# Optimization experiments

Measured on AMD Instinct MI355X. Metric: run time of the kernel, lower is better.

Reference implementation:

```python
import jax, jax.numpy as jnp
import numpy as np

B, S, D, H = 4, 2048, 1024, 16
DH = D // H


def setup_inputs() -> dict:
    key = jax.random.key(0)
    ks = jax.random.split(key, 5)
    std = 1.0 / np.sqrt(D)
    return {
        "x": jax.random.normal(ks[0], (B, S, D), dtype=jnp.float32),
        "mask": jnp.ones((S, S), dtype=bool),  # unused by the original forward
        "Wq": jax.random.normal(ks[1], (D, D), dtype=jnp.float32) * std,
        "Wk": jax.random.normal(ks[2], (D, D), dtype=jnp.float32) * std,
        "Wv": jax.random.normal(ks[3], (D, D), dtype=jnp.float32) * std,
        "Wout": jax.random.normal(ks[4], (D, D), dtype=jnp.float32) * std,
    }


def reference(x, mask, Wq, Wk, Wv, Wout):
    n, s, d = x.shape
    scale = 1.0 / np.sqrt(DH).astype(np.float32)
    q = (x @ Wq).reshape(n, s, H, DH)
    k = (x @ Wk).reshape(n, s, H, DH)
    v = (x @ Wv).reshape(n, s, H, DH)
    # scores [n, q, k, h]; softmax over k axis (dim=-2 in original)
    attn = jnp.einsum('nqhd,nkhd->nqkh', q, k) * scale
    attn = jax.nn.softmax(attn, axis=-2)
    z = jnp.einsum('nqkh,nkhd->nqhd', attn, v).reshape(n, s, d)
    z = jnp.einsum('nqd,de->nqe', z, Wout)
    return x + z
```

## Files before the change

### kernel.cpp

```cpp
#include <hip/hip_runtime.h>

#define Bn 4
#define Sn 2048
#define Dn 1024
#define Hn 16
#define DHn 64

typedef float f32x4 __attribute__((ext_vector_type(4)));
typedef short bf16x8 __attribute__((ext_vector_type(8)));
typedef unsigned short u16;
typedef unsigned int u32;
typedef unsigned short u16x8 __attribute__((ext_vector_type(8)));
typedef unsigned short u16x4 __attribute__((ext_vector_type(4)));
typedef u32 u32x4 __attribute__((ext_vector_type(4)));

union B8 { u32x4 u; bf16x8 s; u16x8 h; };

__device__ __forceinline__ u16 f2bf(float f){
  union { float f; u32 u; } v; v.f = f;
  return (u16)((v.u + 0x7fffu + ((v.u >> 16) & 1u)) >> 16);
}

__device__ __forceinline__ u32 pack_bf2(float lo, float hi){
  union { float f; u32 u; } a, b;
  a.f = lo; b.f = hi;
  return __builtin_amdgcn_perm(b.u, a.u, 0x07060302u);
}

#if __has_builtin(__builtin_amdgcn_exp2f)
#define EXP2(x) __builtin_amdgcn_exp2f(x)
#define QSCALE 0.18033688011112042f
#else
#define EXP2(x) __expf(x)
#define QSCALE 0.125f
#endif

#if __has_builtin(__builtin_amdgcn_global_load_lds)
#define G2L16(l, g) __builtin_amdgcn_global_load_lds((const __attribute__((address_space(1))) u32*)(g), \
                                                     (__attribute__((address_space(3))) u32*)(l), 16, 0, 0)
#else
#define G2L16(l, g) (*(bf16x8*)(l) = *(const bf16x8*)(g))
#endif

__global__ void prep_kernel(const float* __restrict__ x,
                            const float* __restrict__ Wq, const float* __restrict__ Wk,
                            const float* __restrict__ Wv, const float* __restrict__ Wo,
                            u16* __restrict__ xb, u16* __restrict__ wt_all){
  __shared__ u16 tile[64*66];
  const int t = threadIdx.x;
  if (blockIdx.x < 4096){
    size_t i = ((size_t)blockIdx.x * 256 + t) * 8;
    float4 f0 = *(const float4*)(x + i);
    float4 f1 = *(const float4*)(x + i + 4);
    u16x8 o;
    o[0]=f2bf(f0.x); o[1]=f2bf(f0.y); o[2]=f2bf(f0.z); o[3]=f2bf(f0.w);
    o[4]=f2bf(f1.x); o[5]=f2bf(f1.y); o[6]=f2bf(f1.z); o[7]=f2bf(f1.w);
    *(u16x8*)(xb + i) = o;
    return;
  }
  const int wi = blockIdx.x - 4096;
  const int z = wi >> 8, r8 = wi & 255;
  const int k0 = (r8 >> 4) * 64, n0 = (r8 & 15) * 64;
  const float* w = (z == 0) ? Wq : (z == 1) ? Wk : (z == 2) ? Wv : Wo;
  const float scale = (z == 0) ? QSCALE : 1.0f;
  u16* wt = wt_all + (size_t)z * Dn * Dn;
  #pragma unroll
  for (int i = 0; i < 4; i++){
    int idx = i*256 + t;
    int r = idx >> 4, c4 = (idx & 15) * 4;
    float4 f = *(const float4*)(w + (size_t)(k0 + r)*Dn + n0 + c4);
    tile[r*66 + c4 + 0] = f2bf(f.x * scale);
    tile[r*66 + c4 + 1] = f2bf(f.y * scale);
    tile[r*66 + c4 + 2] = f2bf(f.z * scale);
    tile[r*66 + c4 + 3] = f2bf(f.w * scale);
  }
  __syncthreads();
  #pragma unroll
  for (int i = 0; i < 4; i++){
    int idx = i*256 + t;
    int nr = idx >> 4, kc4 = (idx & 15) * 4;
    u16x4 o;
    o[0] = tile[(kc4+0)*66 + nr];
    o[1] = tile[(kc4+1)*66 + nr];
    o[2] = tile[(kc4+2)*66 + nr];
    o[3] = tile[(kc4+3)*66 + nr];
    *(u16x4*)(wt + (size_t)(n0 + nr)*Dn + k0 + kc4) = o;
  }
}

__launch_bounds__(256)
__global__ void gemm_qkv_kernel(const u16* __restrict__ xb, const u16* __restrict__ wt_all,
                                u16* __restrict__ qb, u16* __restrict__ kb, u16* __restrict__ vtb){
  __shared__ u16 smem[32768];
  const int t = threadIdx.x;
  const int wave = t >> 6, lane = t & 63;
  const int ln = lane & 15, quad = lane >> 4;
  const int wm = wave >> 1, wn = wave & 1;
  const int n0 = blockIdx.x * 128;
  const int m0 = blockIdx.y * 128;
  const int zsel = blockIdx.z;
  const u16* wt = wt_all + (size_t)zsel * Dn * Dn;

  f32x4 acc[4][4] = {};

  #pragma unroll
  for (int sub = 0; sub < 2; sub++)
    #pragma unroll
    for (int i = 0; i < 2; i++){
      int idx = i*256 + t;
      int r = idx >> 2, c8 = (idx & 3) * 8;
      G2L16(&smem[sub*8192 + idx*8],        xb + (size_t)(m0 + r)*Dn + sub*32 + c8);
      G2L16(&smem[sub*8192 + 4096 + idx*8], wt + (size_t)(n0 + r)*Dn + sub*32 + c8);
    }

  for (int ki = 0; ki < 16; ki++){
    const int cur = ki & 1;
    __syncthreads();
    if (ki + 1 < 16){
      const int nxt = 16384 * ((ki+1) & 1);
      const int kt = (ki+1) * 64;
      #pragma unroll
      for (int sub = 0; sub < 2; sub++)
        #pragma unroll
        for (int i = 0; i < 2; i++){
          int idx = i*256 + t;
          int r = idx >> 2, c8 = (idx & 3) * 8;
          G2L16(&smem[nxt + sub*8192 + idx*8],        xb + (size_t)(m0 + r)*Dn + kt + sub*32 + c8);
          G2L16(&smem[nxt + sub*8192 + 4096 + idx*8], wt + (size_t)(n0 + r)*Dn + kt + sub*32 + c8);
        }
    }
    #pragma unroll
    for (int sub = 0; sub < 2; sub++){
      const u16* As = &smem[16384*cur + sub*8192];
      const u16* Bs = As + 4096;
      bf16x8 a[4], b[4];
      #pragma unroll
      for (int rb = 0; rb < 4; rb++) a[rb] = *(const bf16x8*)&As[(wm*64 + rb*16 + ln)*32 + quad*8];
      #pragma unroll
      for (int cb = 0; cb < 4; cb++) b[cb] = *(const bf16x8*)&Bs[(wn*64 + cb*16 + ln)*32 + quad*8];
      #pragma unroll
      for (int rb = 0; rb < 4; rb++)
        #pragma unroll
        for (int cb = 0; cb < 4; cb++)
          acc[rb][cb] = __builtin_amdgcn_mfma_f32_16x16x32_bf16(a[rb], b[cb], acc[rb][cb], 0, 0, 0);
    }
  }

  __syncthreads();
  u16* Cs = smem;
  if (zsel < 2){
    #pragma unroll
    for (int rb = 0; rb < 4; rb++)
      #pragma unroll
      for (int cb = 0; cb < 4; cb++)
        #pragma unroll
        for (int reg = 0; reg < 4; reg++)
          Cs[(wm*64 + rb*16 + quad*4 + reg)*136 + wn*64 + cb*16 + ln] = f2bf(acc[rb][cb][reg]);
  } else {
    #pragma unroll
    for (int rb = 0; rb < 4; rb++)
      #pragma unroll
      for (int cb = 0; cb < 4; cb++){
        u16x4 o;
        #pragma unroll
        for (int reg = 0; reg < 4; reg++) o[reg] = f2bf(acc[rb][cb][reg]);
        *(u16x4*)&Cs[(wn*64 + cb*16 + ln)*136 + wm*64 + rb*16 + quad*4] = o;
      }
  }
  __syncthreads();

  if (zsel < 2){
    u16* outp = (zsel == 0) ? qb : kb;
    #pragma unroll
    for (int i = 0; i < 8; i++){
      int idx = i*256 + t;
      int r = idx >> 4, c8 = (idx & 15) * 8;
      bf16x8 vdat = *(const bf16x8*)&Cs[r*136 + c8];
      int row = m0 + r, bb = row >> 11, s = row & 2047;
      int col = n0 + c8, hh = col >> 6, d = col & 63;
      *(bf16x8*)(outp + (((size_t)bb*Hn + hh)*Sn + s)*DHn + d) = vdat;
    }
  } else {
    #pragma unroll
    for (int i = 0; i < 8; i++){
      int idx = i*256 + t;
      int c = idx >> 4, r8 = (idx & 15) * 8;
      bf16x8 vdat = *(const bf16x8*)&Cs[c*136 + r8];
      int col = n0 + c, hh = col >> 6, d = col & 63;
      int row = m0 + r8, bb = row >> 11, s = row & 2047;
      *(bf16x8*)(vtb + (((size_t)bb*Hn + hh)*DHn + d)*Sn + s) = vdat;
    }
  }
}

__launch_bounds__(256, 2)
__global__ void attn_kernel(const u16* q, const u16* __restrict__ k,
                            const u16* __restrict__ vt, u16* z){
  __shared__ u16 Ks[2][64*72];
  __shared__ u16 Vs[2][64*72];
  const int t = threadIdx.x;
  const int wave = t >> 6, lane = t & 63;
  const int ln = lane & 15, quad = lane >> 4;
  const int qt = blockIdx.x, h = blockIdx.y, b = blockIdx.z;
  const size_t bh = (size_t)b * Hn + h;
  const int q0 = qt*256 + wave*64;
  const u16* qp = q + bh * Sn * DHn;
  const u16* kp = k + bh * Sn * DHn;
  const u16* vp = vt + bh * DHn * Sn;

  bf16x8 qf[4][2];
  #pragma unroll
  for (int n = 0; n < 4; n++)
    #pragma unroll
    for (int kq = 0; kq < 2; kq++)
      qf[n][kq] = *(const bf16x8*)(qp + (size_t)(q0 + n*16 + ln)*DHn + kq*32 + quad*8);

  f32x4 zacc[4][4] = {};
  float dacc[4] = {0.f, 0.f, 0.f, 0.f};

  int sr[2], sc[2], vc1[2], vc2[2];
  #pragma unroll
  for (int i = 0; i < 2; i++){
    int idx = i*256 + t, r = idx >> 3, a = idx & 7;
    sr[i] = r; sc[i] = a*8;
    int ksg = a >> 2, q1 = ((a&3)*2)&3, h1 = (a&3) >> 1;
    vc1[i] = ksg*32 + q1*8 + h1*4;
    vc2[i] = ksg*32 + (((q1+1)&3))*8 + h1*4;
  }

  bf16x8 rk[2], rv[2];
  #pragma unroll
  for (int i = 0; i < 2; i++){
    rk[i] = *(const bf16x8*)(kp + (size_t)sr[i]*DHn + sc[i]);
    rv[i] = *(const bf16x8*)(vp + (size_t)sr[i]*Sn + sc[i]);
  }
  #pragma unroll
  for (int i = 0; i < 2; i++){
    *(bf16x8*)&Ks[0][sr[i]*72 + sc[i]] = rk[i];
    u16x4 lo = *(u16x4*)&rv[i];
    u16x4 hi = *((u16x4*)&rv[i] + 1);
    *(u16x4*)&Vs[0][sr[i]*72 + vc1[i]] = lo;
    *(u16x4*)&Vs[0][sr[i]*72 + vc2[i]] = hi;
  }

  for (int kt = 0; kt < Sn/64; kt++){
    const int cur = kt & 1;
    __syncthreads();

    if (kt + 1 < Sn/64){
      #pragma unroll
      for (int i = 0; i < 2; i++){
        rk[i] = *(const bf16x8*)(kp + (size_t)((kt+1)*64 + sr[i])*DHn + sc[i]);
        rv[i] = *(const bf16x8*)(vp + (size_t)sr[i]*Sn + (kt+1)*64 + sc[i]);
      }
    }
    const u16* Kc = Ks[cur];
    const u16* Vc = Vs[cur];

    #pragma unroll
    for (int ks = 0; ks < 2; ks++){
      f32x4 sacc[2][4] = {};
      #pragma unroll
      for (int kq = 0; kq < 2; kq++){
        bf16x8 ka[2];
        #pragma unroll
        for (int m2 = 0; m2 < 2; m2++)
          ka[m2] = *(const bf16x8*)&Kc[((2*ks + m2)*16 + ln)*72 + kq*32 + quad*8];
        #pragma unroll
        for (int m2 = 0; m2 < 2; m2++)
          #pragma unroll
          for (int n = 0; n < 4; n++)
            sacc[m2][n] = __builtin_amdgcn_mfma_f32_16x16x32_bf16(ka[m2], qf[n][kq], sacc[m2][n], 0, 0, 0);
      }
      B8 pb[4];
      #pragma unroll
      for (int n = 0; n < 4; n++){
        f32x4 s0 = sacc[0][n], s1 = sacc[1][n];
        float a0 = EXP2(s0[0]), a1 = EXP2(s0[1]), a2 = EXP2(s0[2]), a3 = EXP2(s0[3]);
        float b0 = EXP2(s1[0]), b1 = EXP2(s1[1]), b2 = EXP2(s1[2]), b3 = EXP2(s1[3]);
        dacc[n] += ((a0 + a1) + (a2 + a3)) + ((b0 + b1) + (b2 + b3));
        pb[n].u = (u32x4){pack_bf2(a0, a1), pack_bf2(a2, a3), pack_bf2(b0, b1), pack_bf2(b2, b3)};
      }
      #pragma unroll
      for (int mtd = 0; mtd < 4; mtd++){
        bf16x8 va = *(const bf16x8*)&Vc[(mtd*16 + ln)*72 + ks*32 + quad*8];
        #pragma unroll
        for (int n = 0; n < 4; n++)
          zacc[mtd][n] = __builtin_amdgcn_mfma_f32_16x16x32_bf16(va, pb[n].s, zacc[mtd][n], 0, 0, 0);
      }
    }

    if (kt + 1 < Sn/64){
      const int nxt = (kt+1) & 1;
      #pragma unroll
      for (int i = 0; i < 2; i++){
        *(bf16x8*)&Ks[nxt][sr[i]*72 + sc[i]] = rk[i];
        u16x4 lo = *(u16x4*)&rv[i];
        u16x4 hi = *((u16x4*)&rv[i] + 1);
        *(u16x4*)&Vs[nxt][sr[i]*72 + vc1[i]] = lo;
        *(u16x4*)&Vs[nxt][sr[i]*72 + vc2[i]] = hi;
      }
    }
  }

  float inv[4];
  #pragma unroll
  for (int n = 0; n < 4; n++){
    float d = dacc[n];
    d += __shfl_xor(d, 16, 64);
    d += __shfl_xor(d, 32, 64);
    inv[n] = 1.0f / d;
  }

  #pragma unroll
  for (int mtd = 0; mtd < 4; mtd++)
    #pragma unroll
    for (int n = 0; n < 4; n++){
      u16x4 o;
      #pragma unroll
      for (int j = 0; j < 4; j++) o[j] = f2bf(zacc[mtd][n][j] * inv[n]);
      *(u16x4*)(z + (bh*Sn + (size_t)(q0 + n*16 + ln))*DHn + mtd*16 + quad*4) = o;
    }
}

__launch_bounds__(256)
__global__ void gemm_out_kernel(const u16* __restrict__ zb, const u16* __restrict__ wt,
                                const float* __restrict__ x, float* __restrict__ out){
  __shared__ u16 smem[32768];
  const int t = threadIdx.x;
  const int wave = t >> 6, lane = t & 63;
  const int ln = lane & 15, quad = lane >> 4;
  const int wm = wave >> 1, wn = wave & 1;
  const int n0 = blockIdx.x * 128;
  const int m0 = blockIdx.y * 128;

  f32x4 acc[4][4] = {};

  #pragma unroll
  for (int sub = 0; sub < 2; sub++)
    #pragma unroll
    for (int i = 0; i < 2; i++){
      int idx = i*256 + t;
      int r = idx >> 2, c8 = (idx & 3) * 8;
      int row = m0 + r, bb = row >> 11, s = row & 2047;
      G2L16(&smem[sub*8192 + idx*8],        zb + (((size_t)bb*Hn + 0)*Sn + s)*DHn + sub*32 + c8);
      G2L16(&smem[sub*8192 + 4096 + idx*8], wt + (size_t)(n0 + r)*Dn + sub*32 + c8);
    }

  for (int ki = 0; ki < 16; ki++){
    const int cur = ki & 1;
    __syncthreads();
    if (ki + 1 < 16){
      const int nxt = 16384 * ((ki+1) & 1);
      const int hh = ki + 1;
      const int kt = (ki+1) * 64;
      #pragma unroll
      for (int sub = 0; sub < 2; sub++)
        #pragma unroll
        for (int i = 0; i < 2; i++){
          int idx = i*256 + t;
          int r = idx >> 2, c8 = (idx & 3) * 8;
          int row = m0 + r, bb = row >> 11, s = row & 2047;
          G2L16(&smem[nxt + sub*8192 + idx*8],        zb + (((size_t)bb*Hn + hh)*Sn + s)*DHn + sub*32 + c8);
          G2L16(&smem[nxt + sub*8192 + 4096 + idx*8], wt + (size_t)(n0 + r)*Dn + kt + sub*32 + c8);
        }
    }
    #pragma unroll
    for (int sub = 0; sub < 2; sub++){
      const u16* As = &smem[16384*cur + sub*8192];
      const u16* Bs = As + 4096;
      bf16x8 a[4], b[4];
      #pragma unroll
      for (int rb = 0; rb < 4; rb++) a[rb] = *(const bf16x8*)&As[(wm*64 + rb*16 + ln)*32 + quad*8];
      #pragma unroll
      for (int cb = 0; cb < 4; cb++) b[cb] = *(const bf16x8*)&Bs[(wn*64 + cb*16 + ln)*32 + quad*8];
      #pragma unroll
      for (int rb = 0; rb < 4; rb++)
        #pragma unroll
        for (int cb = 0; cb < 4; cb++)
          acc[rb][cb] = __builtin_amdgcn_mfma_f32_16x16x32_bf16(a[rb], b[cb], acc[rb][cb], 0, 0, 0);
    }
  }

  #pragma unroll
  for (int rb = 0; rb < 4; rb++)
    #pragma unroll
    for (int cb = 0; cb < 4; cb++)
      #pragma unroll
      for (int reg = 0; reg < 4; reg++){
        int row = m0 + wm*64 + rb*16 + quad*4 + reg;
        int col = n0 + wn*64 + cb*16 + ln;
        size_t off = (size_t)row*Dn + col;
        out[off] = acc[rb][cb][reg] + x[off];
      }
}

extern "C" void kernel_launch(void* const* d_in, const int* in_sizes, int n_in,
                              void* d_out, int out_size, void* d_ws, size_t ws_size,
                              hipStream_t stream){
  const float* x    = (const float*)d_in[0];
  const float* Wq   = (const float*)d_in[2];
  const float* Wk   = (const float*)d_in[3];
  const float* Wv   = (const float*)d_in[4];
  const float* Wout = (const float*)d_in[5];
  float* out = (float*)d_out;

  u16* ws = (u16*)d_ws;
  const size_t NW = (size_t)Dn * Dn;
  const size_t NX = (size_t)Bn * Sn * Dn;
  u16* wt  = ws;
  u16* xb  = wt + 4*NW;
  u16* qb  = xb + NX;
  u16* kb  = qb + NX;
  u16* vtb = kb + NX;

  dim3 blk(256);
  prep_kernel     <<<dim3(4096 + 1024), blk, 0, stream>>>(x, Wq, Wk, Wv, Wout, xb, wt);
  gemm_qkv_kernel <<<dim3(8,64,3), blk, 0, stream>>>(xb, wt, qb, kb, vtb);
  attn_kernel     <<<dim3(8,16,4), blk, 0, stream>>>(qb, kb, vtb, qb);
  gemm_out_kernel <<<dim3(8,64), blk, 0, stream>>>(qb, wt + 3*NW, x, out);
}
```

Baseline: 279.0 us.

## Rewrite QKV GEMM with 256x256 tiles, swizzled LDS and interleaved prefetch schedule

The QKV projection GEMM moves to 512-thread workgroups computing 256x256 output tiles. It uses XOR-swizzled LDS layouts and a hand-scheduled pipeline that interleaves half-tile global-to-LDS loads with MFMA phases, using raw barriers, vmcnt waits and setprio. Workgroup IDs are remapped across XCDs for the QKV, attention and output GEMM kernels to improve L2 locality. The larger tiles cut global traffic per FLOP but raise register and LDS pressure. The manual waitcnt and barrier scheduling is fragile.

```diff
diff --git a/kernel.cpp b/kernel.cpp
--- a/kernel.cpp
+++ b/kernel.cpp
@@ -88,107 +88,193 @@
   }
 }
 
-__launch_bounds__(256)
+#define MFMA_B16(d, va, vb) (d) = __builtin_amdgcn_mfma_f32_16x16x32_bf16((va), (vb), (d), 0, 0, 0)
+#define BARRAW() __builtin_amdgcn_s_barrier()
+#define WAIT_LGKM0() asm volatile("s_waitcnt lgkmcnt(0)" ::: "memory")
+#define VM6() asm volatile("s_waitcnt vmcnt(6)" ::: "memory")
+#define VM0() asm volatile("s_waitcnt vmcnt(0)" ::: "memory")
+#define SCHEDB() __builtin_amdgcn_sched_barrier(0)
+
+__launch_bounds__(512, 2)
 __global__ void gemm_qkv_kernel(const u16* __restrict__ xb, const u16* __restrict__ wt_all,
                                 u16* __restrict__ qb, u16* __restrict__ kb, u16* __restrict__ vtb){
-  __shared__ u16 smem[32768];
+  __shared__ u16 sm[65536];
   const int t = threadIdx.x;
-  const int wave = t >> 6, lane = t & 63;
+  const int lane = t & 63, wave = t >> 6;
   const int ln = lane & 15, quad = lane >> 4;
-  const int wm = wave >> 1, wn = wave & 1;
-  const int n0 = blockIdx.x * 128;
-  const int m0 = blockIdx.y * 128;
-  const int zsel = blockIdx.z;
+  const int wm = wave >> 2, wn = wave & 3;
+
+  const int lin = blockIdx.x;
+  const int wg = (lin & 7) * 48 + (lin >> 3);
+  const int zsel = wg >> 7;
+  const int rem = wg & 127;
+  const int m0 = (rem >> 2) * 256;
+  const int n0 = (rem & 3) * 256;
   const u16* wt = wt_all + (size_t)zsel * Dn * Dn;
 
-  f32x4 acc[4][4] = {};
-
-  #pragma unroll
-  for (int sub = 0; sub < 2; sub++)
-    #pragma unroll
-    for (int i = 0; i < 2; i++){
-      int idx = i*256 + t;
-      int r = idx >> 2, c8 = (idx & 3) * 8;
-      G2L16(&smem[sub*8192 + idx*8],        xb + (size_t)(m0 + r)*Dn + sub*32 + c8);
-      G2L16(&smem[sub*8192 + 4096 + idx*8], wt + (size_t)(n0 + r)*Dn + sub*32 + c8);
-    }
-
-  for (int ki = 0; ki < 16; ki++){
-    const int cur = ki & 1;
-    __syncthreads();
-    if (ki + 1 < 16){
-      const int nxt = 16384 * ((ki+1) & 1);
-      const int kt = (ki+1) * 64;
-      #pragma unroll
-      for (int sub = 0; sub < 2; sub++)
-        #pragma unroll
-        for (int i = 0; i < 2; i++){
-          int idx = i*256 + t;
-          int r = idx >> 2, c8 = (idx & 3) * 8;
-          G2L16(&smem[nxt + sub*8192 + idx*8],        xb + (size_t)(m0 + r)*Dn + kt + sub*32 + c8);
-          G2L16(&smem[nxt + sub*8192 + 4096 + idx*8], wt + (size_t)(n0 + r)*Dn + kt + sub*32 + c8);
+  const int r0 = t >> 3,      sg0 = (t & 7) ^ (r0 & 7);
+  const int i1 = 512 + t;
+  const int r1 = i1 >> 3,     sg1 = (i1 & 7) ^ (r1 & 7);
+  const u16* ax0 = xb + (size_t)(m0 + r0)*Dn + sg0*8;
+  const u16* ax1 = xb + (size_t)(m0 + r1)*Dn + sg1*8;
+  const u16* bw0 = wt + (size_t)(n0 + r0)*Dn + sg0*8;
+  const u16* bw1 = wt + (size_t)(n0 + r1)*Dn + sg1*8;
+  const int ld0 = t*8, ld1 = 4096 + t*8;
+
+#define STG_A(buf, h, tt) do { \
+    G2L16(&sm[(buf)*32768 + (h)*8192 + ld0], ax0 + (size_t)(h)*128*Dn + (tt)*64); \
+    G2L16(&sm[(buf)*32768 + (h)*8192 + ld1], ax1 + (size_t)(h)*128*Dn + (tt)*64); } while(0)
+#define STG_B(buf, h, tt) do { \
+    G2L16(&sm[(buf)*32768 + 16384 + (h)*8192 + ld0], bw0 + (size_t)(h)*128*Dn + (tt)*64); \
+    G2L16(&sm[(buf)*32768 + 16384 + (h)*8192 + ld1], bw1 + (size_t)(h)*128*Dn + (tt)*64); } while(0)
+
+  const int swz = (ln & 7) * 8;
+  const int ac0 = (quad*8) ^ swz;
+  const int ac1 = (32 + quad*8) ^ swz;
+  const int abase = wm*8192 + ln*64;
+  const int bbase = 16384 + (wn>>1)*8192 + ((wn&1)*64 + ln)*64;
+
+  f32x4 acc[8][4] = {};
+  bf16x8 aq[4][2], bq[4][2];
+
+  STG_B(0,0,0); STG_B(0,1,0); STG_A(0,0,0); STG_A(0,1,0);
+  STG_B(1,0,1); STG_B(1,1,1); STG_A(1,0,1);
+  VM6();
+  BARRAW();
+
+  for (int tp = 0; tp < 16; tp += 2){
+    #pragma unroll
+    for (int pi2 = 0; pi2 < 2; pi2++){
+      const int tt = tp + pi2;
+      const int cur = pi2;
+      const int nxt = cur ^ 1;
+      const u16* bufp = &sm[cur*32768];
+
+      #pragma unroll
+      for (int i = 0; i < 4; i++){
+        aq[i][0] = *(const bf16x8*)&bufp[abase + i*1024 + ac0];
+        aq[i][1] = *(const bf16x8*)&bufp[abase + i*1024 + ac1];
+      }
+      #pragma unroll
+      for (int nf = 0; nf < 4; nf++){
+        bq[nf][0] = *(const bf16x8*)&bufp[bbase + nf*1024 + ac0];
+        bq[nf][1] = *(const bf16x8*)&bufp[bbase + nf*1024 + ac1];
+      }
+      SCHEDB();
+      if (tt + 1 < 16) STG_A(nxt, 1, tt+1);
+      BARRAW();
+      WAIT_LGKM0();
+      __builtin_amdgcn_s_setprio(1);
+      #pragma unroll
+      for (int i = 0; i < 4; i++)
+        #pragma unroll
+        for (int nf = 0; nf < 2; nf++){
+          MFMA_B16(acc[i][nf], aq[i][0], bq[nf][0]);
+          MFMA_B16(acc[i][nf], aq[i][1], bq[nf][1]);
         }
-    }
-    #pragma unroll
-    for (int sub = 0; sub < 2; sub++){
-      const u16* As = &smem[16384*cur + sub*8192];
-      const u16* Bs = As + 4096;
-      bf16x8 a[4], b[4];
-      #pragma unroll
-      for (int rb = 0; rb < 4; rb++) a[rb] = *(const bf16x8*)&As[(wm*64 + rb*16 + ln)*32 + quad*8];
-      #pragma unroll
-      for (int cb = 0; cb < 4; cb++) b[cb] = *(const bf16x8*)&Bs[(wn*64 + cb*16 + ln)*32 + quad*8];
-      #pragma unroll
-      for (int rb = 0; rb < 4; rb++)
-        #pragma unroll
-        for (int cb = 0; cb < 4; cb++)
-          acc[rb][cb] = __builtin_amdgcn_mfma_f32_16x16x32_bf16(a[rb], b[cb], acc[rb][cb], 0, 0, 0);
-    }
-  }
-
-  __syncthreads();
-  u16* Cs = smem;
-  if (zsel < 2){
-    #pragma unroll
-    for (int rb = 0; rb < 4; rb++)
-      #pragma unroll
-      for (int cb = 0; cb < 4; cb++)
-        #pragma unroll
-        for (int reg = 0; reg < 4; reg++)
-          Cs[(wm*64 + rb*16 + quad*4 + reg)*136 + wn*64 + cb*16 + ln] = f2bf(acc[rb][cb][reg]);
-  } else {
-    #pragma unroll
-    for (int rb = 0; rb < 4; rb++)
-      #pragma unroll
-      for (int cb = 0; cb < 4; cb++){
-        u16x4 o;
-        #pragma unroll
-        for (int reg = 0; reg < 4; reg++) o[reg] = f2bf(acc[rb][cb][reg]);
-        *(u16x4*)&Cs[(wn*64 + cb*16 + ln)*136 + wm*64 + rb*16 + quad*4] = o;
-      }
-  }
-  __syncthreads();
-
+      __builtin_amdgcn_s_setprio(0);
+      BARRAW();
+
+      if (tt + 2 < 16) STG_B(cur, 0, tt+2);
+      BARRAW();
+      __builtin_amdgcn_s_setprio(1);
+      #pragma unroll
+      for (int i = 0; i < 4; i++)
+        #pragma unroll
+        for (int nf = 2; nf < 4; nf++){
+          MFMA_B16(acc[i][nf], aq[i][0], bq[nf][0]);
+          MFMA_B16(acc[i][nf], aq[i][1], bq[nf][1]);
+        }
+      __builtin_amdgcn_s_setprio(0);
+      BARRAW();
+
+      #pragma unroll
+      for (int i = 0; i < 4; i++){
+        aq[i][0] = *(const bf16x8*)&bufp[abase + (4+i)*1024 + ac0];
+        aq[i][1] = *(const bf16x8*)&bufp[abase + (4+i)*1024 + ac1];
+      }
+      SCHEDB();
+      if (tt + 2 < 16) STG_B(cur, 1, tt+2);
+      BARRAW();
+      WAIT_LGKM0();
+      __builtin_amdgcn_s_setprio(1);
+      #pragma unroll
+      for (int i = 0; i < 4; i++)
+        #pragma unroll
+        for (int nf = 2; nf < 4; nf++){
+          MFMA_B16(acc[4+i][nf], aq[i][0], bq[nf][0]);
+          MFMA_B16(acc[4+i][nf], aq[i][1], bq[nf][1]);
+        }
+      __builtin_amdgcn_s_setprio(0);
+      BARRAW();
+
+      if (tt + 2 < 16) STG_A(cur, 0, tt+2);
+      BARRAW();
+      __builtin_amdgcn_s_setprio(1);
+      #pragma unroll
+      for (int i = 0; i < 4; i++)
+        #pragma unroll
+        for (int nf = 0; nf < 2; nf++){
+          MFMA_B16(acc[4+i][nf], aq[i][0], bq[nf][0]);
+          MFMA_B16(acc[4+i][nf], aq[i][1], bq[nf][1]);
+        }
+      __builtin_amdgcn_s_setprio(0);
+      if (tt + 2 < 16) { VM6(); } else { VM0(); }
+      BARRAW();
+    }
+  }
+
+  u16* Cs = sm;
   if (zsel < 2){
     u16* outp = (zsel == 0) ? qb : kb;
     #pragma unroll
-    for (int i = 0; i < 8; i++){
-      int idx = i*256 + t;
-      int r = idx >> 4, c8 = (idx & 15) * 8;
-      bf16x8 vdat = *(const bf16x8*)&Cs[r*136 + c8];
-      int row = m0 + r, bb = row >> 11, s = row & 2047;
-      int col = n0 + c8, hh = col >> 6, d = col & 63;
-      *(bf16x8*)(outp + (((size_t)bb*Hn + hh)*Sn + s)*DHn + d) = vdat;
+    for (int round = 0; round < 2; round++){
+      if (wm == round){
+        #pragma unroll
+        for (int mf = 0; mf < 8; mf++)
+          #pragma unroll
+          for (int nf = 0; nf < 4; nf++)
+            #pragma unroll
+            for (int reg = 0; reg < 4; reg++)
+              Cs[(mf*16 + quad*4 + reg)*264 + wn*64 + nf*16 + ln] = f2bf(acc[mf][nf][reg]);
+      }
+      __syncthreads();
+      #pragma unroll
+      for (int it = 0; it < 8; it++){
+        int idx = it*512 + t;
+        int r = idx >> 5, c8 = (idx & 31) * 8;
+        bf16x8 vdat = *(const bf16x8*)&Cs[r*264 + c8];
+        int row = m0 + round*128 + r, bb = row >> 11, s = row & 2047;
+        int col = n0 + c8, hh = col >> 6, d = col & 63;
+        *(bf16x8*)(outp + (((size_t)bb*Hn + hh)*Sn + s)*DHn + d) = vdat;
+      }
+      if (round == 0) __syncthreads();
     }
   } else {
     #pragma unroll
-    for (int i = 0; i < 8; i++){
-      int idx = i*256 + t;
-      int c = idx >> 4, r8 = (idx & 15) * 8;
-      bf16x8 vdat = *(const bf16x8*)&Cs[c*136 + r8];
-      int col = n0 + c, hh = col >> 6, d = col & 63;
-      int row = m0 + r8, bb = row >> 11, s = row & 2047;
-      *(bf16x8*)(vtb + (((size_t)bb*Hn + hh)*DHn + d)*Sn + s) = vdat;
+    for (int round = 0; round < 2; round++){
+      if ((wn >> 1) == round){
+        #pragma unroll
+        for (int mf = 0; mf < 8; mf++)
+          #pragma unroll
+          for (int nf = 0; nf < 4; nf++){
+            u16x4 o;
+            #pragma unroll
+            for (int reg = 0; reg < 4; reg++) o[reg] = f2bf(acc[mf][nf][reg]);
+            *(u16x4*)&Cs[((wn&1)*64 + nf*16 + ln)*264 + wm*128 + mf*16 + quad*4] = o;
+          }
+      }
+      __syncthreads();
+      #pragma unroll
+      for (int it = 0; it < 8; it++){
+        int idx = it*512 + t;
+        int r = idx >> 5, c8 = (idx & 31) * 8;
+        bf16x8 vdat = *(const bf16x8*)&Cs[r*264 + c8];
+        int col = n0 + round*128 + r, hh = col >> 6, d = col & 63;
+        int row = m0 + c8, bb = row >> 11, s = row & 2047;
+        *(bf16x8*)(vtb + (((size_t)bb*Hn + hh)*DHn + d)*Sn + s) = vdat;
+      }
+      if (round == 0) __syncthreads();
     }
   }
 }
@@ -201,7 +287,9 @@
   const int t = threadIdx.x;
   const int wave = t >> 6, lane = t & 63;
   const int ln = lane & 15, quad = lane >> 4;
-  const int qt = blockIdx.x, h = blockIdx.y, b = blockIdx.z;
+  const int lin = blockIdx.x + 8*(blockIdx.y + 16*blockIdx.z);
+  const int wgs = (lin & 7)*64 + (lin >> 3);
+  const int qt = wgs & 7, h = (wgs >> 3) & 15, b = wgs >> 7;
   const size_t bh = (size_t)b * Hn + h;
   const int q0 = qt*256 + wave*64;
   const u16* qp = q + bh * Sn * DHn;
@@ -331,8 +419,10 @@
   const int wave = t >> 6, lane = t & 63;
   const int ln = lane & 15, quad = lane >> 4;
   const int wm = wave >> 1, wn = wave & 1;
-  const int n0 = blockIdx.x * 128;
-  const int m0 = blockIdx.y * 128;
+  const int lin = blockIdx.y * 8 + blockIdx.x;
+  const int wgs = (lin & 7)*64 + (lin >> 3);
+  const int n0 = (wgs & 7) * 128;
+  const int m0 = (wgs >> 3) * 128;
 
   f32x4 acc[4][4] = {};
 
@@ -414,9 +504,8 @@
   u16* kb  = qb + NX;
   u16* vtb = kb + NX;
 
-  dim3 blk(256);
-  prep_kernel     <<<dim3(4096 + 1024), blk, 0, stream>>>(x, Wq, Wk, Wv, Wout, xb, wt);
-  gemm_qkv_kernel <<<dim3(8,64,3), blk, 0, stream>>>(xb, wt, qb, kb, vtb);
-  attn_kernel     <<<dim3(8,16,4), blk, 0, stream>>>(qb, kb, vtb, qb);
-  gemm_out_kernel <<<dim3(8,64), blk, 0, stream>>>(qb, wt + 3*NW, x, out);
-}
+  prep_kernel     <<<dim3(4096 + 1024), dim3(256), 0, stream>>>(x, Wq, Wk, Wv, Wout, xb, wt);
+  gemm_qkv_kernel <<<dim3(384), dim3(512), 0, stream>>>(xb, wt, qb, kb, vtb);
+  attn_kernel     <<<dim3(8,16,4), dim3(256), 0, stream>>>(qb, kb, vtb, qb);
+  gemm_out_kernel <<<dim3(8,64), dim3(256), 0, stream>>>(qb, wt + 3*NW, x, out);
+}
```

New measurement: 263.7 us. 1.06x faster.

## Rework GEMM pipelines with swizzled LDS, triple buffering, and XCD-aware block remapping

Applied to the files above, without the earlier changes.

Both projection GEMMs are rewritten so the A tile is triple-buffered and the B tile double-buffered in LDS. Loads use an XOR-swizzled 64-wide layout to avoid bank conflicts. Explicit vmcnt/lgkmcnt waits, raw barriers, sched_barriers and setprio interleave the global-to-LDS prefetch with the MFMA work. Block indices for the GEMMs and the attention kernel are remapped so consecutive workgroups land on the same XCD, aiming for better L2 reuse. The hand-written wait counts and barriers are fragile and raise LDS use per block.

```diff
diff --git a/kernel.cpp b/kernel.cpp
--- a/kernel.cpp
+++ b/kernel.cpp
@@ -41,6 +41,13 @@
 #else
 #define G2L16(l, g) (*(bf16x8*)(l) = *(const bf16x8*)(g))
 #endif
+
+#define MFMA_B16(d, va, vb) (d) = __builtin_amdgcn_mfma_f32_16x16x32_bf16((va), (vb), (d), 0, 0, 0)
+#define BARRAW() __builtin_amdgcn_s_barrier()
+#define WAIT_LGKM0() asm volatile("s_waitcnt lgkmcnt(0)" ::: "memory")
+#define VM4() asm volatile("s_waitcnt vmcnt(4)" ::: "memory")
+#define VM0() asm volatile("s_waitcnt vmcnt(0)" ::: "memory")
+#define SCHEDB() __builtin_amdgcn_sched_barrier(0)
 
 __global__ void prep_kernel(const float* __restrict__ x,
                             const float* __restrict__ Wq, const float* __restrict__ Wk,
@@ -91,64 +98,106 @@
 __launch_bounds__(256)
 __global__ void gemm_qkv_kernel(const u16* __restrict__ xb, const u16* __restrict__ wt_all,
                                 u16* __restrict__ qb, u16* __restrict__ kb, u16* __restrict__ vtb){
-  __shared__ u16 smem[32768];
+  __shared__ u16 sm[40960];
   const int t = threadIdx.x;
-  const int wave = t >> 6, lane = t & 63;
+  const int lane = t & 63, wave = t >> 6;
   const int ln = lane & 15, quad = lane >> 4;
   const int wm = wave >> 1, wn = wave & 1;
-  const int n0 = blockIdx.x * 128;
-  const int m0 = blockIdx.y * 128;
-  const int zsel = blockIdx.z;
+
+  const int lin = blockIdx.x;
+  const int wg = (lin & 7) * 192 + (lin >> 3);
+  const int zsel = wg >> 9;
+  const int rem = wg & 511;
+  const int m0 = (rem >> 3) * 128;
+  const int n0 = (rem & 7) * 128;
   const u16* wt = wt_all + (size_t)zsel * Dn * Dn;
 
+  const u16* ap[4]; const u16* bp[4]; int ldo[4];
+  #pragma unroll
+  for (int p = 0; p < 4; p++){
+    int idx = p*256 + t;
+    int r = idx >> 3, g = (idx & 7) ^ (r & 7);
+    ap[p] = xb + (size_t)(m0 + r)*Dn + g*8;
+    bp[p] = wt + (size_t)(n0 + r)*Dn + g*8;
+    ldo[p] = idx * 8;
+  }
+#define STGA(buf, tt) do { _Pragma("unroll") for (int p = 0; p < 4; p++) \
+    G2L16(&sm[(buf) + ldo[p]], ap[p] + (size_t)(tt)*64); } while(0)
+#define STGB(buf, tt) do { _Pragma("unroll") for (int p = 0; p < 4; p++) \
+    G2L16(&sm[(buf) + ldo[p]], bp[p] + (size_t)(tt)*64); } while(0)
+
+  const int agr0 = ((    quad) ^ (ln & 7)) * 8;
+  const int agr1 = ((4 + quad) ^ (ln & 7)) * 8;
+  int arow[4], brow[4];
+  #pragma unroll
+  for (int i = 0; i < 4; i++) arow[i] = (wm*64 + i*16 + ln) * 64;
+  #pragma unroll
+  for (int j = 0; j < 4; j++) brow[j] = (wn*64 + j*16 + ln) * 64;
+
   f32x4 acc[4][4] = {};
 
-  #pragma unroll
-  for (int sub = 0; sub < 2; sub++)
+  STGA(0, 0); STGB(24576, 0); STGA(8192, 1);
+
+  #pragma unroll
+  for (int tt = 0; tt < 16; ++tt){
+    const int a_cur = (tt % 3) * 8192;
+    const int a_pf  = ((tt + 2) % 3) * 8192;
+    const int b_cur = 24576 + (tt & 1) * 8192;
+    const int b_pf  = 24576 + ((tt + 1) & 1) * 8192;
+
+    if (tt < 15) { VM4(); } else { VM0(); }
+    BARRAW(); SCHEDB();
+
+    bf16x8 a01[2][2], bq[4][2];
     #pragma unroll
     for (int i = 0; i < 2; i++){
-      int idx = i*256 + t;
-      int r = idx >> 2, c8 = (idx & 3) * 8;
-      G2L16(&smem[sub*8192 + idx*8],        xb + (size_t)(m0 + r)*Dn + sub*32 + c8);
-      G2L16(&smem[sub*8192 + 4096 + idx*8], wt + (size_t)(n0 + r)*Dn + sub*32 + c8);
-    }
-
-  for (int ki = 0; ki < 16; ki++){
-    const int cur = ki & 1;
-    __syncthreads();
-    if (ki + 1 < 16){
-      const int nxt = 16384 * ((ki+1) & 1);
-      const int kt = (ki+1) * 64;
-      #pragma unroll
-      for (int sub = 0; sub < 2; sub++)
-        #pragma unroll
-        for (int i = 0; i < 2; i++){
-          int idx = i*256 + t;
-          int r = idx >> 2, c8 = (idx & 3) * 8;
-          G2L16(&smem[nxt + sub*8192 + idx*8],        xb + (size_t)(m0 + r)*Dn + kt + sub*32 + c8);
-          G2L16(&smem[nxt + sub*8192 + 4096 + idx*8], wt + (size_t)(n0 + r)*Dn + kt + sub*32 + c8);
-        }
-    }
-    #pragma unroll
-    for (int sub = 0; sub < 2; sub++){
-      const u16* As = &smem[16384*cur + sub*8192];
-      const u16* Bs = As + 4096;
-      bf16x8 a[4], b[4];
-      #pragma unroll
-      for (int rb = 0; rb < 4; rb++) a[rb] = *(const bf16x8*)&As[(wm*64 + rb*16 + ln)*32 + quad*8];
-      #pragma unroll
-      for (int cb = 0; cb < 4; cb++) b[cb] = *(const bf16x8*)&Bs[(wn*64 + cb*16 + ln)*32 + quad*8];
-      #pragma unroll
-      for (int rb = 0; rb < 4; rb++)
-        #pragma unroll
-        for (int cb = 0; cb < 4; cb++)
-          acc[rb][cb] = __builtin_amdgcn_mfma_f32_16x16x32_bf16(a[rb], b[cb], acc[rb][cb], 0, 0, 0);
-    }
+      a01[i][0] = *(const bf16x8*)&sm[a_cur + arow[i] + agr0];
+      a01[i][1] = *(const bf16x8*)&sm[a_cur + arow[i] + agr1];
+    }
+    #pragma unroll
+    for (int j = 0; j < 4; j++){
+      bq[j][0] = *(const bf16x8*)&sm[b_cur + brow[j] + agr0];
+      bq[j][1] = *(const bf16x8*)&sm[b_cur + brow[j] + agr1];
+    }
+    SCHEDB();
+    if (tt < 15) STGB(b_pf, tt + 1);
+    SCHEDB();
+    WAIT_LGKM0(); SCHEDB();
+    __builtin_amdgcn_s_setprio(1);
+    #pragma unroll
+    for (int i = 0; i < 2; i++)
+      #pragma unroll
+      for (int j = 0; j < 4; j++){
+        MFMA_B16(acc[i][j], a01[i][0], bq[j][0]);
+        MFMA_B16(acc[i][j], a01[i][1], bq[j][1]);
+      }
+    __builtin_amdgcn_s_setprio(0);
+
+    bf16x8 a23[2][2];
+    #pragma unroll
+    for (int i = 0; i < 2; i++){
+      a23[i][0] = *(const bf16x8*)&sm[a_cur + arow[2+i] + agr0];
+      a23[i][1] = *(const bf16x8*)&sm[a_cur + arow[2+i] + agr1];
+    }
+    SCHEDB();
+    if (tt < 14) STGA(a_pf, tt + 2);
+    SCHEDB();
+    WAIT_LGKM0(); SCHEDB();
+    __builtin_amdgcn_s_setprio(1);
+    #pragma unroll
+    for (int i = 0; i < 2; i++)
+      #pragma unroll
+      for (int j = 0; j < 4; j++){
+        MFMA_B16(acc[2+i][j], a23[i][0], bq[j][0]);
+        MFMA_B16(acc[2+i][j], a23[i][1], bq[j][1]);
+      }
+    __builtin_amdgcn_s_setprio(0);
   }
 
   __syncthreads();
-  u16* Cs = smem;
+  u16* Cs = sm;
   if (zsel < 2){
+    u16* outp = (zsel == 0) ? qb : kb;
     #pragma unroll
     for (int rb = 0; rb < 4; rb++)
       #pragma unroll
@@ -156,21 +205,7 @@
         #pragma unroll
         for (int reg = 0; reg < 4; reg++)
           Cs[(wm*64 + rb*16 + quad*4 + reg)*136 + wn*64 + cb*16 + ln] = f2bf(acc[rb][cb][reg]);
-  } else {
-    #pragma unroll
-    for (int rb = 0; rb < 4; rb++)
-      #pragma unroll
-      for (int cb = 0; cb < 4; cb++){
-        u16x4 o;
-        #pragma unroll
-        for (int reg = 0; reg < 4; reg++) o[reg] = f2bf(acc[rb][cb][reg]);
-        *(u16x4*)&Cs[(wn*64 + cb*16 + ln)*136 + wm*64 + rb*16 + quad*4] = o;
-      }
-  }
-  __syncthreads();
-
-  if (zsel < 2){
-    u16* outp = (zsel == 0) ? qb : kb;
+    __syncthreads();
     #pragma unroll
     for (int i = 0; i < 8; i++){
       int idx = i*256 + t;
@@ -182,6 +217,16 @@
     }
   } else {
     #pragma unroll
+    for (int rb = 0; rb < 4; rb++)
+      #pragma unroll
+      for (int cb = 0; cb < 4; cb++){
+        u16x4 o;
+        #pragma unroll
+        for (int reg = 0; reg < 4; reg++) o[reg] = f2bf(acc[rb][cb][reg]);
+        *(u16x4*)&Cs[(wn*64 + cb*16 + ln)*136 + wm*64 + rb*16 + quad*4] = o;
+      }
+    __syncthreads();
+    #pragma unroll
     for (int i = 0; i < 8; i++){
       int idx = i*256 + t;
       int c = idx >> 4, r8 = (idx & 15) * 8;
@@ -191,6 +236,8 @@
       *(bf16x8*)(vtb + (((size_t)bb*Hn + hh)*DHn + d)*Sn + s) = vdat;
     }
   }
+#undef STGA
+#undef STGB
 }
 
 __launch_bounds__(256, 2)
@@ -201,7 +248,9 @@
   const int t = threadIdx.x;
   const int wave = t >> 6, lane = t & 63;
   const int ln = lane & 15, quad = lane >> 4;
-  const int qt = blockIdx.x, h = blockIdx.y, b = blockIdx.z;
+  const int lin = blockIdx.x + 8*(blockIdx.y + 16*blockIdx.z);
+  const int wgs = (lin & 7)*64 + (lin >> 3);
+  const int qt = wgs & 7, h = (wgs >> 3) & 15, b = wgs >> 7;
   const size_t bh = (size_t)b * Hn + h;
   const int q0 = qt*256 + wave*64;
   const u16* qp = q + bh * Sn * DHn;
@@ -326,60 +375,97 @@
 __launch_bounds__(256)
 __global__ void gemm_out_kernel(const u16* __restrict__ zb, const u16* __restrict__ wt,
                                 const float* __restrict__ x, float* __restrict__ out){
-  __shared__ u16 smem[32768];
+  __shared__ u16 sm[40960];
   const int t = threadIdx.x;
-  const int wave = t >> 6, lane = t & 63;
+  const int lane = t & 63, wave = t >> 6;
   const int ln = lane & 15, quad = lane >> 4;
   const int wm = wave >> 1, wn = wave & 1;
-  const int n0 = blockIdx.x * 128;
-  const int m0 = blockIdx.y * 128;
+
+  const int lin = blockIdx.x;
+  const int wg = (lin & 7) * 64 + (lin >> 3);
+  const int m0 = (wg >> 3) * 128;
+  const int n0 = (wg & 7) * 128;
+
+  const u16* ap[4]; const u16* bp[4]; int ldo[4];
+  #pragma unroll
+  for (int p = 0; p < 4; p++){
+    int idx = p*256 + t;
+    int r = idx >> 3, g = (idx & 7) ^ (r & 7);
+    int row = m0 + r, bb = row >> 11, s = row & 2047;
+    ap[p] = zb + ((size_t)bb*Hn*Sn + s)*DHn + g*8;
+    bp[p] = wt + (size_t)(n0 + r)*Dn + g*8;
+    ldo[p] = idx * 8;
+  }
+#define STGA(buf, tt) do { _Pragma("unroll") for (int p = 0; p < 4; p++) \
+    G2L16(&sm[(buf) + ldo[p]], ap[p] + (size_t)(tt)*Sn*DHn); } while(0)
+#define STGB(buf, tt) do { _Pragma("unroll") for (int p = 0; p < 4; p++) \
+    G2L16(&sm[(buf) + ldo[p]], bp[p] + (size_t)(tt)*64); } while(0)
+
+  const int agr0 = ((    quad) ^ (ln & 7)) * 8;
+  const int agr1 = ((4 + quad) ^ (ln & 7)) * 8;
+  int arow[4], brow[4];
+  #pragma unroll
+  for (int i = 0; i < 4; i++) arow[i] = (wm*64 + i*16 + ln) * 64;
+  #pragma unroll
+  for (int j = 0; j < 4; j++) brow[j] = (wn*64 + j*16 + ln) * 64;
 
   f32x4 acc[4][4] = {};
-
-  #pragma unroll
-  for (int sub = 0; sub < 2; sub++)
+  STGA(0, 0); STGB(24576, 0); STGA(8192, 1);
+
+  #pragma unroll
+  for (int tt = 0; tt < 16; ++tt){
+    const int a_cur = (tt % 3) * 8192;
+    const int a_pf  = ((tt + 2) % 3) * 8192;
+    const int b_cur = 24576 + (tt & 1) * 8192;
+    const int b_pf  = 24576 + ((tt + 1) & 1) * 8192;
+
+    if (tt < 15) { VM4(); } else { VM0(); }
+    BARRAW(); SCHEDB();
+
+    bf16x8 a01[2][2], bq[4][2];
     #pragma unroll
     for (int i = 0; i < 2; i++){
-      int idx = i*256 + t;
-      int r = idx >> 2, c8 = (idx & 3) * 8;
-      int row = m0 + r, bb = row >> 11, s = row & 2047;
-      G2L16(&smem[sub*8192 + idx*8],        zb + (((size_t)bb*Hn + 0)*Sn + s)*DHn + sub*32 + c8);
-      G2L16(&smem[sub*8192 + 4096 + idx*8], wt + (size_t)(n0 + r)*Dn + sub*32 + c8);
-    }
-
-  for (int ki = 0; ki < 16; ki++){
-    const int cur = ki & 1;
-    __syncthreads();
-    if (ki + 1 < 16){
-      const int nxt = 16384 * ((ki+1) & 1);
-      const int hh = ki + 1;
-      const int kt = (ki+1) * 64;
-      #pragma unroll
-      for (int sub = 0; sub < 2; sub++)
-        #pragma unroll
-        for (int i = 0; i < 2; i++){
-          int idx = i*256 + t;
-          int r = idx >> 2, c8 = (idx & 3) * 8;
-          int row = m0 + r, bb = row >> 11, s = row & 2047;
-          G2L16(&smem[nxt + sub*8192 + idx*8],        zb + (((size_t)bb*Hn + hh)*Sn + s)*DHn + sub*32 + c8);
-          G2L16(&smem[nxt + sub*8192 + 4096 + idx*8], wt + (size_t)(n0 + r)*Dn + kt + sub*32 + c8);
-        }
-    }
-    #pragma unroll
-    for (int sub = 0; sub < 2; sub++){
-      const u16* As = &smem[16384*cur + sub*8192];
-      const u16* Bs = As + 4096;
-      bf16x8 a[4], b[4];
-      #pragma unroll
-      for (int rb = 0; rb < 4; rb++) a[rb] = *(const bf16x8*)&As[(wm*64 + rb*16 + ln)*32 + quad*8];
-      #pragma unroll
-      for (int cb = 0; cb < 4; cb++) b[cb] = *(const bf16x8*)&Bs[(wn*64 + cb*16 + ln)*32 + quad*8];
-      #pragma unroll
-      for (int rb = 0; rb < 4; rb++)
-        #pragma unroll
-        for (int cb = 0; cb < 4; cb++)
-          acc[rb][cb] = __builtin_amdgcn_mfma_f32_16x16x32_bf16(a[rb], b[cb], acc[rb][cb], 0, 0, 0);
-    }
+      a01[i][0] = *(const bf16x8*)&sm[a_cur + arow[i] + agr0];
+      a01[i][1] = *(const bf16x8*)&sm[a_cur + arow[i] + agr1];
+    }
+    #pragma unroll
+    for (int j = 0; j < 4; j++){
+      bq[j][0] = *(const bf16x8*)&sm[b_cur + brow[j] + agr0];
+      bq[j][1] = *(const bf16x8*)&sm[b_cur + brow[j] + agr1];
+    }
+    SCHEDB();
+    if (tt < 15) STGB(b_pf, tt + 1);
+    SCHEDB();
+    WAIT_LGKM0(); SCHEDB();
+    __builtin_amdgcn_s_setprio(1);
+    #pragma unroll
+    for (int i = 0; i < 2; i++)
+      #pragma unroll
+      for (int j = 0; j < 4; j++){
+        MFMA_B16(acc[i][j], a01[i][0], bq[j][0]);
+        MFMA_B16(acc[i][j], a01[i][1], bq[j][1]);
+      }
+    __builtin_amdgcn_s_setprio(0);
+
+    bf16x8 a23[2][2];
+    #pragma unroll
+    for (int i = 0; i < 2; i++){
+      a23[i][0] = *(const bf16x8*)&sm[a_cur + arow[2+i] + agr0];
+      a23[i][1] = *(const bf16x8*)&sm[a_cur + arow[2+i] + agr1];
+    }
+    SCHEDB();
+    if (tt < 14) STGA(a_pf, tt + 2);
+    SCHEDB();
+    WAIT_LGKM0(); SCHEDB();
+    __builtin_amdgcn_s_setprio(1);
+    #pragma unroll
+    for (int i = 0; i < 2; i++)
+      #pragma unroll
+      for (int j = 0; j < 4; j++){
+        MFMA_B16(acc[2+i][j], a23[i][0], bq[j][0]);
+        MFMA_B16(acc[2+i][j], a23[i][1], bq[j][1]);
+      }
+    __builtin_amdgcn_s_setprio(0);
   }
 
   #pragma unroll
@@ -393,6 +479,8 @@
         size_t off = (size_t)row*Dn + col;
         out[off] = acc[rb][cb][reg] + x[off];
       }
+#undef STGA
+#undef STGB
 }
 
 extern "C" void kernel_launch(void* const* d_in, const int* in_sizes, int n_in,
@@ -414,9 +502,8 @@
   u16* kb  = qb + NX;
   u16* vtb = kb + NX;
 
-  dim3 blk(256);
-  prep_kernel     <<<dim3(4096 + 1024), blk, 0, stream>>>(x, Wq, Wk, Wv, Wout, xb, wt);
-  gemm_qkv_kernel <<<dim3(8,64,3), blk, 0, stream>>>(xb, wt, qb, kb, vtb);
-  attn_kernel     <<<dim3(8,16,4), blk, 0, stream>>>(qb, kb, vtb, qb);
-  gemm_out_kernel <<<dim3(8,64), blk, 0, stream>>>(qb, wt + 3*NW, x, out);
-}
+  prep_kernel     <<<dim3(4096 + 1024), dim3(256), 0, stream>>>(x, Wq, Wk, Wv, Wout, xb, wt);
+  gemm_qkv_kernel <<<dim3(1536), dim3(256), 0, stream>>>(xb, wt, qb, kb, vtb);
+  attn_kernel     <<<dim3(8,16,4), dim3(256), 0, stream>>>(qb, kb, vtb, qb);
+  gemm_out_kernel <<<dim3(512), dim3(256), 0, stream>>>(qb, wt + 3*NW, x, out);
+}
```

Result: faster. 255.2 us (-8.6%).
